# Performance work log

Measured on AMD Instinct MI355X. Metric: run time of the kernel, lower is better.

## Reference

```python
import jax, jax.numpy as jnp
import numpy as np

N = 50000
E = 400000
IN_FEATS = 256
HIDDEN = 64
HEADS = 8
CLASSES = 40
NEG_SLOPE = 0.2  # DGL GATConv default negative_slope


def setup_inputs() -> dict:
    key = jax.random.key(0)
    ks = jax.random.split(key, 12)
    features = jax.random.normal(ks[0], (N, IN_FEATS), dtype=jnp.float32)
    src = jax.random.randint(ks[1], (E,), 0, N, dtype=jnp.int32)
    dst = jax.random.randint(ks[2], (E,), 0, N, dtype=jnp.int32)
    s = 0.05
    # layer 0: in_feats -> HEADS*HIDDEN
    W1 = jax.random.normal(ks[3], (IN_FEATS, HEADS * HIDDEN), dtype=jnp.float32) * s
    al1 = jax.random.normal(ks[4], (HEADS, HIDDEN), dtype=jnp.float32) * s
    ar1 = jax.random.normal(ks[5], (HEADS, HIDDEN), dtype=jnp.float32) * s
    # layer 1: HEADS*HIDDEN -> HEADS*HIDDEN
    W2 = jax.random.normal(ks[6], (HEADS * HIDDEN, HEADS * HIDDEN), dtype=jnp.float32) * s
    al2 = jax.random.normal(ks[7], (HEADS, HIDDEN), dtype=jnp.float32) * s
    ar2 = jax.random.normal(ks[8], (HEADS, HIDDEN), dtype=jnp.float32) * s
    # layer 2: HEADS*HIDDEN -> 1*CLASSES
    W3 = jax.random.normal(ks[9], (HEADS * HIDDEN, CLASSES), dtype=jnp.float32) * s
    al3 = jax.random.normal(ks[10], (1, CLASSES), dtype=jnp.float32) * s
    ar3 = jax.random.normal(ks[11], (1, CLASSES), dtype=jnp.float32) * s
    return {"features": features, "src": src, "dst": dst,
            "W1": W1, "al1": al1, "ar1": ar1,
            "W2": W2, "al2": al2, "ar2": ar2,
            "W3": W3, "al3": al3, "ar3": ar3}


def gat_conv(h, W, al, ar, src, dst):
    """DGL GATConv (no bias, no residual, no activation, no dropout)."""
    H, D = al.shape
    feat = (h @ W).reshape(N, H, D)                      # [N,H,D]
    el = jnp.sum(feat * al[None], axis=-1)               # [N,H]
    er = jnp.sum(feat * ar[None], axis=-1)               # [N,H]
    e = jax.nn.leaky_relu(el[src] + er[dst], NEG_SLOPE)  # [E,H]
    # edge softmax over incoming edges of each dst node
    m = jax.ops.segment_max(e, dst, num_segments=N)      # [N,H]
    ex = jnp.exp(e - m[dst])                             # [E,H]
    denom = jax.ops.segment_sum(ex, dst, num_segments=N) # [N,H]
    alpha = ex / denom[dst]                              # [E,H]
    msg = alpha[:, :, None] * feat[src]                  # [E,H,D]
    out = jax.ops.segment_sum(msg, dst, num_segments=N)  # [N,H,D]
    return out.reshape(N, H * D)


def reference(features, src, dst, W1, al1, ar1, W2, al2, ar2, W3, al3, ar3):
    h = gat_conv(features, W1, al1, ar1, src, dst)  # [N, HEADS*HIDDEN]
    h = gat_conv(h, W2, al2, ar2, src, dst)         # [N, HEADS*HIDDEN]
    h = gat_conv(h, W3, al3, ar3, src, dst)         # [N, CLASSES]
    return h
```

## Files before the change

kernel.cpp:

```cpp
#include <hip/hip_runtime.h>
#include <hip/hip_bf16.h>

#define NN 50000
#define NE 400000
#define MPAD 50048
#define SLOTS 48

typedef __bf16 bf16x8_t __attribute__((ext_vector_type(8)));
typedef __bf16 bf16x4_t __attribute__((ext_vector_type(4)));
typedef float f32x4_t __attribute__((ext_vector_type(4)));

__device__ __forceinline__ float bhi(unsigned int u) {
    union { unsigned int i; float f; } v; v.i = u & 0xffff0000u; return v.f;
}
__device__ __forceinline__ float blo(unsigned int u) {
    union { unsigned int i; float f; } v; v.i = u << 16; return v.f;
}

__global__ __launch_bounds__(256) void prep_kernel(
    const float* __restrict__ W1, __hip_bfloat16* __restrict__ W1t,
    const float* __restrict__ W2, __hip_bfloat16* __restrict__ W2t,
    const float* __restrict__ W3, __hip_bfloat16* __restrict__ W3t,
    const float* __restrict__ al1, const float* __restrict__ ar1,
    const float* __restrict__ al2, const float* __restrict__ ar2,
    __hip_bfloat16* __restrict__ walr1, __hip_bfloat16* __restrict__ walr2) {
    int stride = gridDim.x * blockDim.x;
    for (int i = blockIdx.x * blockDim.x + threadIdx.x; i < 512 * 512; i += stride) {
        if (i < 512 * 256) {
            int n = i >> 8, k = i & 255;
            W1t[i] = __float2bfloat16(W1[k * 512 + n]);
        }
        {
            int n = i >> 9, k = i & 511;
            W2t[i] = __float2bfloat16(W2[k * 512 + n]);
        }
        if (i < 48 * 512) {
            int n = i >> 9, k = i & 511;
            W3t[i] = __float2bfloat16((n < 40) ? W3[k * 40 + n] : 0.f);
        }
        if (i < 16 * 256) {
            int j = i >> 8, k = i & 255;
            const float* v = (j < 8) ? (al1 + j * 64) : (ar1 + (j - 8) * 64);
            float s = 0.f;
            for (int d = 0; d < 64; ++d) s += W1[(size_t)k * 512 + (j & 7) * 64 + d] * v[d];
            walr1[(k >> 5) * 512 + j * 32 + (k & 31)] = __float2bfloat16(s);
        }
        if (i < 16 * 512) {
            int j = i >> 9, k = i & 511;
            const float* v = (j < 8) ? (al2 + j * 64) : (ar2 + (j - 8) * 64);
            float s = 0.f;
            for (int d = 0; d < 64; ++d) s += W2[(size_t)k * 512 + (j & 7) * 64 + d] * v[d];
            walr2[(k >> 5) * 512 + j * 32 + (k & 31)] = __float2bfloat16(s);
        }
    }
}

__global__ void build_kernel(const int* __restrict__ src, const int* __restrict__ dst,
                             int* __restrict__ deg, int* __restrict__ slot) {
    int e = blockIdx.x * blockDim.x + threadIdx.x;
    if (e < NE) {
        int d = dst[e];
        int p = atomicAdd(&deg[d], 1);
        if (p < SLOTS) slot[(size_t)d * SLOTS + p] = src[e];
    }
}

__global__ __launch_bounds__(256) void cast_kernel(const float* __restrict__ f,
                                                   __hip_bfloat16* __restrict__ o) {
    int i = blockIdx.x * 256 + threadIdx.x;
    const float* p = f + (size_t)i * 8;
    float4 a = *reinterpret_cast<const float4*>(p);
    float4 b = *reinterpret_cast<const float4*>(p + 4);
    bf16x8_t h;
    h[0] = (__bf16)a.x; h[1] = (__bf16)a.y; h[2] = (__bf16)a.z; h[3] = (__bf16)a.w;
    h[4] = (__bf16)b.x; h[5] = (__bf16)b.y; h[6] = (__bf16)b.z; h[7] = (__bf16)b.w;
    *reinterpret_cast<bf16x8_t*>(o + (size_t)i * 8) = h;
}

__device__ __forceinline__ void gld_lds16(const void* g, void* l) {
    __builtin_amdgcn_global_load_lds(
        (const __attribute__((address_space(1))) unsigned int*)g,
        (__attribute__((address_space(3))) unsigned int*)l, 16, 0, 0);
}

template <int K>
__global__ __launch_bounds__(256, 2) void gemm_all(const __hip_bfloat16* __restrict__ A,
                                                   const __hip_bfloat16* __restrict__ Wt,
                                                   const __hip_bfloat16* __restrict__ walr,
                                                   __hip_bfloat16* __restrict__ C,
                                                   float* __restrict__ el,
                                                   float* __restrict__ er) {
    const int NT = K / 32;
    __shared__ __align__(16) char smem[2 * 36864];
    const int w = threadIdx.x >> 6;
    const int lane = threadIdx.x & 63;
    const int quad = lane >> 4, l15 = lane & 15;
    const int row0 = blockIdx.x * 64;
    const int srow = lane >> 2;
    const int csrc = ((lane & 3) ^ ((lane >> 3) & 3)) * 8;
    const int rswz = l15 * 64 + ((quad ^ ((l15 >> 1) & 3)) << 4);

    const __hip_bfloat16* gA = A + (size_t)(row0 + w * 16 + srow) * K + csrc;
    const __hip_bfloat16* gBb = Wt + (size_t)(w * 128 + srow) * K + csrc;

    f32x4_t acc[4][8] = {};
    f32x4_t acce[4] = {};

    {
        char* buf = smem;
        gld_lds16(gA, buf + w * 1024);
#pragma unroll
        for (int o = 0; o < 8; ++o)
            gld_lds16(gBb + (size_t)o * 16 * K, buf + 4096 + (w * 8 + o) * 1024);
    }

#pragma unroll
    for (int t = 0; t < NT; ++t) {
        char* buf = smem + (t & 1) * 36864;
        bf16x8_t b5;
        if (w == 0) {
            b5 = *reinterpret_cast<const bf16x8_t*>(walr + t * 512 + l15 * 32 + quad * 8);
            asm volatile("" ::: "memory");
        }
        if (t + 1 < NT) {
            char* nb = smem + ((t + 1) & 1) * 36864;
            const int k1 = (t + 1) * 32;
            gld_lds16(gA + k1, nb + w * 1024);
#pragma unroll
            for (int o = 0; o < 8; ++o)
                gld_lds16(gBb + (size_t)o * 16 * K + k1, nb + 4096 + (w * 8 + o) * 1024);
            asm volatile("s_waitcnt vmcnt(9)" ::: "memory");
        } else {
            asm volatile("s_waitcnt vmcnt(0)" ::: "memory");
        }
        __builtin_amdgcn_s_barrier();
        asm volatile("" ::: "memory");
        bf16x8_t a[4], b[8];
#pragma unroll
        for (int mi = 0; mi < 4; mi++)
            a[mi] = *reinterpret_cast<const bf16x8_t*>(buf + mi * 1024 + rswz);
#pragma unroll
        for (int ni = 0; ni < 8; ni++)
            b[ni] = *reinterpret_cast<const bf16x8_t*>(buf + 4096 + (w * 8 + ni) * 1024 + rswz);
#pragma unroll
        for (int mi = 0; mi < 4; mi++)
#pragma unroll
            for (int ni = 0; ni < 8; ni++)
                acc[mi][ni] = __builtin_amdgcn_mfma_f32_16x16x32_bf16(a[mi], b[ni], acc[mi][ni], 0, 0, 0);
        if (w == 0) {
#pragma unroll
            for (int mi = 0; mi < 4; mi++)
                acce[mi] = __builtin_amdgcn_mfma_f32_16x16x32_bf16(a[mi], b5, acce[mi], 0, 0, 0);
        }
        asm volatile("" ::: "memory");
        __builtin_amdgcn_s_barrier();
        asm volatile("" ::: "memory");
    }

#pragma unroll
    for (int mi = 0; mi < 4; mi++) {
#pragma unroll
        for (int ni = 0; ni < 8; ni++) {
#pragma unroll
            for (int r = 0; r < 4; r++) {
                int row = row0 + mi * 16 + quad * 4 + r;
                if (row < NN)
                    C[(size_t)row * 512 + w * 128 + ni * 16 + l15] =
                        __float2bfloat16(acc[mi][ni][r]);
            }
        }
    }
    if (w == 0) {
#pragma unroll
        for (int mi = 0; mi < 4; mi++) {
#pragma unroll
            for (int r = 0; r < 4; r++) {
                int row = row0 + mi * 16 + quad * 4 + r;
                if (row < NN) {
                    float v = acce[mi][r];
                    if (l15 < 8) el[row * 8 + l15] = v;
                    else er[row * 8 + l15 - 8] = v;
                }
            }
        }
    }
}

#define W3_LDSROW 520
__global__ __launch_bounds__(256) void gemm3_mfma(const __hip_bfloat16* __restrict__ A,
                                                  const __hip_bfloat16* __restrict__ W3t,
                                                  const float* __restrict__ al,
                                                  const float* __restrict__ ar,
                                                  __hip_bfloat16* __restrict__ C,
                                                  float* __restrict__ el,
                                                  float* __restrict__ er) {
    __shared__ __align__(16) __hip_bfloat16 wlds[48 * W3_LDSROW];
    for (int c = threadIdx.x; c < 48 * 64; c += 256) {
        int n = c >> 6, koff = (c & 63) * 8;
        *reinterpret_cast<uint4*>(&wlds[n * W3_LDSROW + koff]) =
            *reinterpret_cast<const uint4*>(W3t + n * 512 + koff);
    }
    __syncthreads();
    const int w = threadIdx.x >> 6;
    const int lane = threadIdx.x & 63;
    const int quad = lane >> 4, l15 = lane & 15;
    const int row0 = blockIdx.x * 64 + w * 16;

    float alv[3], arv[3];
#pragma unroll
    for (int c = 0; c < 3; c++) {
        int col = c * 16 + l15;
        alv[c] = (col < 40) ? al[col] : 0.f;
        arv[c] = (col < 40) ? ar[col] : 0.f;
    }

    f32x4_t acc[3] = {};
    const __hip_bfloat16* arow = A + (size_t)(row0 + l15) * 512;
#pragma unroll 4
    for (int k0 = 0; k0 < 512; k0 += 32) {
        bf16x8_t a = *reinterpret_cast<const bf16x8_t*>(arow + k0 + quad * 8);
#pragma unroll
        for (int c = 0; c < 3; c++) {
            bf16x8_t b = *reinterpret_cast<const bf16x8_t*>(
                &wlds[(c * 16 + l15) * W3_LDSROW + k0 + quad * 8]);
            acc[c] = __builtin_amdgcn_mfma_f32_16x16x32_bf16(a, b, acc[c], 0, 0, 0);
        }
    }
#pragma unroll
    for (int r = 0; r < 4; r++) {
        int row = row0 + quad * 4 + r;
        bool rok = row < NN;
        float pl = 0.f, pr = 0.f;
#pragma unroll
        for (int c = 0; c < 3; c++) {
            float v = acc[c][r];
            if (rok) C[(size_t)row * 64 + c * 16 + l15] = __float2bfloat16(v);
            pl += v * alv[c];
            pr += v * arv[c];
        }
        if (rok) C[(size_t)row * 64 + 48 + l15] = __float2bfloat16(0.f);
        pl += __shfl_xor(pl, 1, 64); pr += __shfl_xor(pr, 1, 64);
        pl += __shfl_xor(pl, 2, 64); pr += __shfl_xor(pr, 2, 64);
        pl += __shfl_xor(pl, 4, 64); pr += __shfl_xor(pr, 4, 64);
        pl += __shfl_xor(pl, 8, 64); pr += __shfl_xor(pr, 8, 64);
        if (l15 == 0 && rok) { el[row] = pl; er[row] = pr; }
    }
}

__device__ __forceinline__ void fma8(float* acc, float pj, const uint4& q) {
    acc[0] += pj * blo(q.x); acc[1] += pj * bhi(q.x);
    acc[2] += pj * blo(q.y); acc[3] += pj * bhi(q.y);
    acc[4] += pj * blo(q.z); acc[5] += pj * bhi(q.z);
    acc[6] += pj * blo(q.w); acc[7] += pj * bhi(q.w);
}

__global__ __launch_bounds__(256) void agg8_kernel(const __hip_bfloat16* __restrict__ feat,
                                                   const float* __restrict__ el,
                                                   const float* __restrict__ er,
                                                   const int* __restrict__ deg,
                                                   const int* __restrict__ slot,
                                                   __hip_bfloat16* __restrict__ out) {
    int n = (blockIdx.x * blockDim.x + threadIdx.x) >> 6;
    int lane = threadIdx.x & 63;
    if (n >= NN) return;
    const int es = lane >> 3;
    const int h8 = lane & 7;
    const int hd = lane >> 3;
    int dn = min(deg[n], SLOTS);
    float er_n = er[n * 8 + h8];
    const int* sl = slot + (size_t)n * SLOTS;

    float lsum = 0.f;
    float acc[8] = {};
    for (int base = 0; base < dn; base += 8) {
        int e = base + es;
        bool valid = e < dn;
        int s = valid ? sl[e] : 0;
        float t = el[s * 8 + h8] + er_n;
        float x = (t >= 0.f) ? t : 0.2f * t;
        float p = valid ? __expf(x) : 0.f;
        lsum += p;
        int cnt = min(8, dn - base);
        int j = 0;
        for (; j + 4 <= cnt; j += 4) {
            int s0 = __builtin_amdgcn_readlane(s, (j + 0) * 8);
            int s1 = __builtin_amdgcn_readlane(s, (j + 1) * 8);
            int s2 = __builtin_amdgcn_readlane(s, (j + 2) * 8);
            int s3 = __builtin_amdgcn_readlane(s, (j + 3) * 8);
            float p0 = __shfl(p, (j + 0) * 8 + hd, 64);
            float p1 = __shfl(p, (j + 1) * 8 + hd, 64);
            float p2 = __shfl(p, (j + 2) * 8 + hd, 64);
            float p3 = __shfl(p, (j + 3) * 8 + hd, 64);
            uint4 q0 = *reinterpret_cast<const uint4*>(feat + (size_t)s0 * 512 + lane * 8);
            uint4 q1 = *reinterpret_cast<const uint4*>(feat + (size_t)s1 * 512 + lane * 8);
            uint4 q2 = *reinterpret_cast<const uint4*>(feat + (size_t)s2 * 512 + lane * 8);
            uint4 q3 = *reinterpret_cast<const uint4*>(feat + (size_t)s3 * 512 + lane * 8);
            fma8(acc, p0, q0);
            fma8(acc, p1, q1);
            fma8(acc, p2, q2);
            fma8(acc, p3, q3);
        }
        for (; j < cnt; ++j) {
            int sj = __builtin_amdgcn_readlane(s, j * 8);
            float pj = __shfl(p, j * 8 + hd, 64);
            uint4 q = *reinterpret_cast<const uint4*>(feat + (size_t)sj * 512 + lane * 8);
            fma8(acc, pj, q);
        }
    }
    lsum += __shfl_xor(lsum, 8, 64);
    lsum += __shfl_xor(lsum, 16, 64);
    lsum += __shfl_xor(lsum, 32, 64);
    float lh = __shfl(lsum, hd, 64);
    float inv = (lh > 0.f) ? 1.f / lh : 0.f;
    bf16x8_t o8;
#pragma unroll
    for (int d = 0; d < 8; ++d) o8[d] = (__bf16)(acc[d] * inv);
    *reinterpret_cast<bf16x8_t*>(out + (size_t)n * 512 + lane * 8) = o8;
}

__global__ __launch_bounds__(256) void agg3_kernel(const __hip_bfloat16* __restrict__ feat,
                                                   const float* __restrict__ el,
                                                   const float* __restrict__ er,
                                                   const int* __restrict__ deg,
                                                   const int* __restrict__ slot,
                                                   float* __restrict__ out) {
    int n = (blockIdx.x * blockDim.x + threadIdx.x) >> 6;
    int lane = threadIdx.x & 63;
    if (n >= NN) return;
    const int es = lane >> 3;
    const int dc = lane & 7;
    int dn = min(deg[n], SLOTS);
    float er_n = er[n];
    const int* sl = slot + (size_t)n * SLOTS;

    float lsum = 0.f;
    float acc[8] = {};
    for (int base = 0; base < dn; base += 16) {
        int e0 = base + es, e1 = base + 8 + es;
        bool v0 = e0 < dn, v1 = e1 < dn;
        int s0 = v0 ? sl[e0] : 0;
        int s1 = v1 ? sl[e1] : 0;
        float t0 = el[s0] + er_n;
        float t1 = el[s1] + er_n;
        float x0 = (t0 >= 0.f) ? t0 : 0.2f * t0;
        float x1 = (t1 >= 0.f) ? t1 : 0.2f * t1;
        float p0 = v0 ? __expf(x0) : 0.f;
        float p1 = v1 ? __expf(x1) : 0.f;
        lsum += p0 + p1;
        uint4 q0 = *reinterpret_cast<const uint4*>(feat + (size_t)s0 * 64 + dc * 8);
        uint4 q1 = *reinterpret_cast<const uint4*>(feat + (size_t)s1 * 64 + dc * 8);
        acc[0] += p0 * blo(q0.x) + p1 * blo(q1.x);
        acc[1] += p0 * bhi(q0.x) + p1 * bhi(q1.x);
        acc[2] += p0 * blo(q0.y) + p1 * blo(q1.y);
        acc[3] += p0 * bhi(q0.y) + p1 * bhi(q1.y);
        acc[4] += p0 * blo(q0.z) + p1 * blo(q1.z);
        acc[5] += p0 * bhi(q0.z) + p1 * bhi(q1.z);
        acc[6] += p0 * blo(q0.w) + p1 * blo(q1.w);
        acc[7] += p0 * bhi(q0.w) + p1 * bhi(q1.w);
    }
    lsum += __shfl_xor(lsum, 8, 64);
    lsum += __shfl_xor(lsum, 16, 64);
    lsum += __shfl_xor(lsum, 32, 64);
#pragma unroll
    for (int d = 0; d < 8; ++d) {
        acc[d] += __shfl_xor(acc[d], 8, 64);
        acc[d] += __shfl_xor(acc[d], 16, 64);
        acc[d] += __shfl_xor(acc[d], 32, 64);
    }
    float inv = (lsum > 0.f) ? 1.f / lsum : 0.f;
    if (es == 0 && dc < 5) {
        float4 o0 = make_float4(acc[0] * inv, acc[1] * inv, acc[2] * inv, acc[3] * inv);
        float4 o1 = make_float4(acc[4] * inv, acc[5] * inv, acc[6] * inv, acc[7] * inv);
        *reinterpret_cast<float4*>(out + (size_t)n * 40 + dc * 8) = o0;
        *reinterpret_cast<float4*>(out + (size_t)n * 40 + dc * 8 + 4) = o1;
    }
}

extern "C" void kernel_launch(void* const* d_in, const int* in_sizes, int n_in,
                              void* d_out, int out_size, void* d_ws, size_t ws_size,
                              hipStream_t stream) {
    const float* features = (const float*)d_in[0];
    const int* src = (const int*)d_in[1];
    const int* dst = (const int*)d_in[2];
    const float* W1 = (const float*)d_in[3];
    const float* al1 = (const float*)d_in[4];
    const float* ar1 = (const float*)d_in[5];
    const float* W2 = (const float*)d_in[6];
    const float* al2 = (const float*)d_in[7];
    const float* ar2 = (const float*)d_in[8];
    const float* W3 = (const float*)d_in[9];
    const float* al3 = (const float*)d_in[10];
    const float* ar3 = (const float*)d_in[11];

    char* ws = (char*)d_ws;
    size_t o = 0;
    auto carve = [&](size_t bytes) -> void* {
        o = (o + 255) & ~(size_t)255;
        void* p = ws + o;
        o += bytes;
        return p;
    };
    __hip_bfloat16* Fbf = (__hip_bfloat16*)carve((size_t)MPAD * 512 * 2);
    __hip_bfloat16* Gbf = (__hip_bfloat16*)carve((size_t)MPAD * 512 * 2);
    __hip_bfloat16* W1t = (__hip_bfloat16*)carve((size_t)512 * 256 * 2);
    __hip_bfloat16* W2t = (__hip_bfloat16*)carve((size_t)512 * 512 * 2);
    __hip_bfloat16* W3t = (__hip_bfloat16*)carve((size_t)48 * 512 * 2);
    __hip_bfloat16* walr1 = (__hip_bfloat16*)carve((size_t)16 * 256 * 2);
    __hip_bfloat16* walr2 = (__hip_bfloat16*)carve((size_t)16 * 512 * 2);
    float* el = (float*)carve((size_t)NN * 8 * 4);
    float* er = (float*)carve((size_t)NN * 8 * 4);
    float* el3 = (float*)carve((size_t)NN * 4);
    float* er3 = (float*)carve((size_t)NN * 4);
    int* deg = (int*)carve((size_t)NN * 4);
    int* slot = (int*)carve((size_t)NN * SLOTS * 4);

    hipMemsetAsync(deg, 0, (size_t)NN * 4, stream);
    build_kernel<<<(NE + 255) / 256, 256, 0, stream>>>(src, dst, deg, slot);
    prep_kernel<<<512, 256, 0, stream>>>(W1, W1t, W2, W2t, W3, W3t,
                                         al1, ar1, al2, ar2, walr1, walr2);

    const int gmm = MPAD / 64;
    cast_kernel<<<(NN * 256 / 8) / 256, 256, 0, stream>>>(features, Gbf);
    gemm_all<256><<<gmm, 256, 0, stream>>>(Gbf, W1t, walr1, Fbf, el, er);
    agg8_kernel<<<(NN + 3) / 4, 256, 0, stream>>>(Fbf, el, er, deg, slot, Gbf);
    gemm_all<512><<<gmm, 256, 0, stream>>>(Gbf, W2t, walr2, Fbf, el, er);
    agg8_kernel<<<(NN + 3) / 4, 256, 0, stream>>>(Fbf, el, er, deg, slot, Gbf);
    gemm3_mfma<<<MPAD / 64, 256, 0, stream>>>(Gbf, W3t, al3, ar3, Fbf, el3, er3);
    agg3_kernel<<<(NN + 3) / 4, 256, 0, stream>>>(Fbf, el3, er3, deg, slot, (float*)d_out);
}
```

Measured before the change: 398.9 us.

## Fuse fp32-to-bf16 cast into first GEMM and restructure agg8 gathers

Removes the separate cast kernel: the first-layer GEMM now loads fp32 features directly, converts them to bf16 in registers and writes the result into shared memory, which saves one full read and write of the feature matrix. The aggregation kernel now loads the slot list once per wavefront and issues all eight neighbour-row gathers up front, before the softmax weights are computed. Padded slots are clamped to the last valid neighbour and given zero weight, which gives more loads in flight at the cost of redundant loads for low-degree nodes. It also adds an early exit for zero-degree nodes and uses nontemporal stores for the output.

```diff
diff --git a/kernel.cpp b/kernel.cpp
--- a/kernel.cpp
+++ b/kernel.cpp
@@ -65,22 +65,128 @@
     }
 }
 
-__global__ __launch_bounds__(256) void cast_kernel(const float* __restrict__ f,
-                                                   __hip_bfloat16* __restrict__ o) {
-    int i = blockIdx.x * 256 + threadIdx.x;
-    const float* p = f + (size_t)i * 8;
-    float4 a = *reinterpret_cast<const float4*>(p);
-    float4 b = *reinterpret_cast<const float4*>(p + 4);
-    bf16x8_t h;
-    h[0] = (__bf16)a.x; h[1] = (__bf16)a.y; h[2] = (__bf16)a.z; h[3] = (__bf16)a.w;
-    h[4] = (__bf16)b.x; h[5] = (__bf16)b.y; h[6] = (__bf16)b.z; h[7] = (__bf16)b.w;
-    *reinterpret_cast<bf16x8_t*>(o + (size_t)i * 8) = h;
-}
-
 __device__ __forceinline__ void gld_lds16(const void* g, void* l) {
     __builtin_amdgcn_global_load_lds(
         (const __attribute__((address_space(1))) unsigned int*)g,
         (__attribute__((address_space(3))) unsigned int*)l, 16, 0, 0);
+}
+
+__global__ __launch_bounds__(256, 2) void gemm1_all(const float* __restrict__ A,
+                                                    const __hip_bfloat16* __restrict__ Wt,
+                                                    const __hip_bfloat16* __restrict__ walr,
+                                                    __hip_bfloat16* __restrict__ C,
+                                                    float* __restrict__ el,
+                                                    float* __restrict__ er) {
+    const int K = 256;
+    const int NT = 8;
+    __shared__ __align__(16) char smem[2 * 36864];
+    const int w = threadIdx.x >> 6;
+    const int lane = threadIdx.x & 63;
+    const int quad = lane >> 4, l15 = lane & 15;
+    const int row0 = blockIdx.x * 64;
+    const int srow = lane >> 2;
+    const int csrc = ((lane & 3) ^ ((lane >> 3) & 3)) * 8;
+    const int rswz = l15 * 64 + ((quad ^ ((l15 >> 1) & 3)) << 4);
+
+    int arow = row0 + w * 16 + srow;
+    int rc = (arow < NN) ? arow : (NN - 1);
+    const float* gA = A + (size_t)rc * K + csrc;
+    const __hip_bfloat16* gBb = Wt + (size_t)(w * 128 + srow) * K + csrc;
+
+    f32x4_t acc[4][8] = {};
+    f32x4_t acce[4] = {};
+    float4 curA0, curA1, nxtA0, nxtA1;
+
+    curA0 = *reinterpret_cast<const float4*>(gA);
+    curA1 = *reinterpret_cast<const float4*>(gA + 4);
+    {
+        char* buf = smem;
+#pragma unroll
+        for (int o = 0; o < 8; ++o)
+            gld_lds16(gBb + (size_t)o * 16 * K, buf + 4096 + (w * 8 + o) * 1024);
+    }
+
+#pragma unroll
+    for (int t = 0; t < NT; ++t) {
+        char* buf = smem + (t & 1) * 36864;
+        bf16x8_t b5;
+        if (w == 0) {
+            b5 = *reinterpret_cast<const bf16x8_t*>(walr + t * 512 + l15 * 32 + quad * 8);
+            asm volatile("" ::: "memory");
+        }
+        if (t + 1 < NT) {
+            char* nb = smem + ((t + 1) & 1) * 36864;
+            const int k1 = (t + 1) * 32;
+            nxtA0 = *reinterpret_cast<const float4*>(gA + k1);
+            nxtA1 = *reinterpret_cast<const float4*>(gA + k1 + 4);
+#pragma unroll
+            for (int o = 0; o < 8; ++o)
+                gld_lds16(gBb + (size_t)o * 16 * K + k1, nb + 4096 + (w * 8 + o) * 1024);
+            asm volatile("s_waitcnt vmcnt(10)" ::: "memory");
+        } else {
+            asm volatile("s_waitcnt vmcnt(0)" ::: "memory");
+        }
+        {
+            bf16x8_t h;
+            h[0] = (__bf16)curA0.x; h[1] = (__bf16)curA0.y;
+            h[2] = (__bf16)curA0.z; h[3] = (__bf16)curA0.w;
+            h[4] = (__bf16)curA1.x; h[5] = (__bf16)curA1.y;
+            h[6] = (__bf16)curA1.z; h[7] = (__bf16)curA1.w;
+            *reinterpret_cast<bf16x8_t*>(buf + w * 1024 + lane * 16) = h;
+        }
+        curA0 = nxtA0; curA1 = nxtA1;
+        asm volatile("s_waitcnt lgkmcnt(0)" ::: "memory");
+        __builtin_amdgcn_s_barrier();
+        asm volatile("" ::: "memory");
+        bf16x8_t a[4], b[8];
+#pragma unroll
+        for (int mi = 0; mi < 4; mi++)
+            a[mi] = *reinterpret_cast<const bf16x8_t*>(buf + mi * 1024 + rswz);
+#pragma unroll
+        for (int ni = 0; ni < 8; ni++)
+            b[ni] = *reinterpret_cast<const bf16x8_t*>(buf + 4096 + (w * 8 + ni) * 1024 + rswz);
+#pragma unroll
+        for (int mi = 0; mi < 4; mi++)
+#pragma unroll
+            for (int ni = 0; ni < 8; ni++)
+                acc[mi][ni] = __builtin_amdgcn_mfma_f32_16x16x32_bf16(a[mi], b[ni], acc[mi][ni], 0, 0, 0);
+        if (w == 0) {
+#pragma unroll
+            for (int mi = 0; mi < 4; mi++)
+                acce[mi] = __builtin_amdgcn_mfma_f32_16x16x32_bf16(a[mi], b5, acce[mi], 0, 0, 0);
+        }
+        asm volatile("" ::: "memory");
+        __builtin_amdgcn_s_barrier();
+        asm volatile("" ::: "memory");
+    }
+
+#pragma unroll
+    for (int mi = 0; mi < 4; mi++) {
+#pragma unroll
+        for (int ni = 0; ni < 8; ni++) {
+#pragma unroll
+            for (int r = 0; r < 4; r++) {
+                int row = row0 + mi * 16 + quad * 4 + r;
+                if (row < NN)
+                    C[(size_t)row * 512 + w * 128 + ni * 16 + l15] =
+                        __float2bfloat16(acc[mi][ni][r]);
+            }
+        }
+    }
+    if (w == 0) {
+#pragma unroll
+        for (int mi = 0; mi < 4; mi++) {
+#pragma unroll
+            for (int r = 0; r < 4; r++) {
+                int row = row0 + mi * 16 + quad * 4 + r;
+                if (row < NN) {
+                    float v = acce[mi][r];
+                    if (l15 < 8) el[row * 8 + l15] = v;
+                    else er[row * 8 + l15 - 8] = v;
+                }
+            }
+        }
+    }
 }
 
 template <int K>
@@ -267,45 +373,51 @@
     const int h8 = lane & 7;
     const int hd = lane >> 3;
     int dn = min(deg[n], SLOTS);
+    __hip_bfloat16* orow = out + (size_t)n * 512 + lane * 8;
+    if (dn == 0) {
+        bf16x8_t z = {};
+        __builtin_nontemporal_store(z, reinterpret_cast<bf16x8_t*>(orow));
+        return;
+    }
     float er_n = er[n * 8 + h8];
     const int* sl = slot + (size_t)n * SLOTS;
+    int slv = sl[lane < dn ? lane : dn - 1];
+    const int dm = dn - 1;
 
     float lsum = 0.f;
     float acc[8] = {};
     for (int base = 0; base < dn; base += 8) {
+        int s0 = __builtin_amdgcn_readlane(slv, min(base + 0, dm));
+        int s1 = __builtin_amdgcn_readlane(slv, min(base + 1, dm));
+        int s2 = __builtin_amdgcn_readlane(slv, min(base + 2, dm));
+        int s3 = __builtin_amdgcn_readlane(slv, min(base + 3, dm));
+        int s4 = __builtin_amdgcn_readlane(slv, min(base + 4, dm));
+        int s5 = __builtin_amdgcn_readlane(slv, min(base + 5, dm));
+        int s6 = __builtin_amdgcn_readlane(slv, min(base + 6, dm));
+        int s7 = __builtin_amdgcn_readlane(slv, min(base + 7, dm));
+        uint4 q0 = *reinterpret_cast<const uint4*>(feat + (size_t)s0 * 512 + lane * 8);
+        uint4 q1 = *reinterpret_cast<const uint4*>(feat + (size_t)s1 * 512 + lane * 8);
+        uint4 q2 = *reinterpret_cast<const uint4*>(feat + (size_t)s2 * 512 + lane * 8);
+        uint4 q3 = *reinterpret_cast<const uint4*>(feat + (size_t)s3 * 512 + lane * 8);
+        uint4 q4 = *reinterpret_cast<const uint4*>(feat + (size_t)s4 * 512 + lane * 8);
+        uint4 q5 = *reinterpret_cast<const uint4*>(feat + (size_t)s5 * 512 + lane * 8);
+        uint4 q6 = *reinterpret_cast<const uint4*>(feat + (size_t)s6 * 512 + lane * 8);
+        uint4 q7 = *reinterpret_cast<const uint4*>(feat + (size_t)s7 * 512 + lane * 8);
         int e = base + es;
         bool valid = e < dn;
-        int s = valid ? sl[e] : 0;
+        int s = __shfl(slv, valid ? e : 0, 64);
         float t = el[s * 8 + h8] + er_n;
         float x = (t >= 0.f) ? t : 0.2f * t;
         float p = valid ? __expf(x) : 0.f;
         lsum += p;
-        int cnt = min(8, dn - base);
-        int j = 0;
-        for (; j + 4 <= cnt; j += 4) {
-            int s0 = __builtin_amdgcn_readlane(s, (j + 0) * 8);
-            int s1 = __builtin_amdgcn_readlane(s, (j + 1) * 8);
-            int s2 = __builtin_amdgcn_readlane(s, (j + 2) * 8);
-            int s3 = __builtin_amdgcn_readlane(s, (j + 3) * 8);
-            float p0 = __shfl(p, (j + 0) * 8 + hd, 64);
-            float p1 = __shfl(p, (j + 1) * 8 + hd, 64);
-            float p2 = __shfl(p, (j + 2) * 8 + hd, 64);
-            float p3 = __shfl(p, (j + 3) * 8 + hd, 64);
-            uint4 q0 = *reinterpret_cast<const uint4*>(feat + (size_t)s0 * 512 + lane * 8);
-            uint4 q1 = *reinterpret_cast<const uint4*>(feat + (size_t)s1 * 512 + lane * 8);
-            uint4 q2 = *reinterpret_cast<const uint4*>(feat + (size_t)s2 * 512 + lane * 8);
-            uint4 q3 = *reinterpret_cast<const uint4*>(feat + (size_t)s3 * 512 + lane * 8);
-            fma8(acc, p0, q0);
-            fma8(acc, p1, q1);
-            fma8(acc, p2, q2);
-            fma8(acc, p3, q3);
-        }
-        for (; j < cnt; ++j) {
-            int sj = __builtin_amdgcn_readlane(s, j * 8);
-            float pj = __shfl(p, j * 8 + hd, 64);
-            uint4 q = *reinterpret_cast<const uint4*>(feat + (size_t)sj * 512 + lane * 8);
-            fma8(acc, pj, q);
-        }
+        float p0 = __shfl(p, 0 * 8 + hd, 64); fma8(acc, p0, q0);
+        float p1 = __shfl(p, 1 * 8 + hd, 64); fma8(acc, p1, q1);
+        float p2 = __shfl(p, 2 * 8 + hd, 64); fma8(acc, p2, q2);
+        float p3 = __shfl(p, 3 * 8 + hd, 64); fma8(acc, p3, q3);
+        float p4 = __shfl(p, 4 * 8 + hd, 64); fma8(acc, p4, q4);
+        float p5 = __shfl(p, 5 * 8 + hd, 64); fma8(acc, p5, q5);
+        float p6 = __shfl(p, 6 * 8 + hd, 64); fma8(acc, p6, q6);
+        float p7 = __shfl(p, 7 * 8 + hd, 64); fma8(acc, p7, q7);
     }
     lsum += __shfl_xor(lsum, 8, 64);
     lsum += __shfl_xor(lsum, 16, 64);
@@ -315,7 +427,7 @@
     bf16x8_t o8;
 #pragma unroll
     for (int d = 0; d < 8; ++d) o8[d] = (__bf16)(acc[d] * inv);
-    *reinterpret_cast<bf16x8_t*>(out + (size_t)n * 512 + lane * 8) = o8;
+    __builtin_nontemporal_store(o8, reinterpret_cast<bf16x8_t*>(orow));
 }
 
 __global__ __launch_bounds__(256) void agg3_kernel(const __hip_bfloat16* __restrict__ feat,
@@ -420,8 +532,7 @@
                                          al1, ar1, al2, ar2, walr1, walr2);
 
     const int gmm = MPAD / 64;
-    cast_kernel<<<(NN * 256 / 8) / 256, 256, 0, stream>>>(features, Gbf);
-    gemm_all<256><<<gmm, 256, 0, stream>>>(Gbf, W1t, walr1, Fbf, el, er);
+    gemm1_all<<<gmm, 256, 0, stream>>>(features, W1t, walr1, Fbf, el, er);
     agg8_kernel<<<(NN + 3) / 4, 256, 0, stream>>>(Fbf, el, er, deg, slot, Gbf);
     gemm_all<512><<<gmm, 256, 0, stream>>>(Gbf, W2t, walr2, Fbf, el, er);
     agg8_kernel<<<(NN + 3) / 4, 256, 0, stream>>>(Fbf, el, er, deg, slot, Gbf);
```

Result: no change. 404.4 us (+1.4%).
